# Kernel optimization log

Measured on AMD Instinct MI355X. Metric: run time of the kernel, lower is better.

## Reference

```python
import jax, jax.numpy as jnp
import numpy as np

ALPHA = 0.2  # leakyrelu negative slope

def setup_inputs() -> dict:
    key = jax.random.key(0)
    k1, k2, k3 = jax.random.split(key, 3)
    N, F_in, F_out = 8192, 512, 256
    input_x = jax.random.normal(k1, (N, F_in), dtype=jnp.float32)
    # xavier-ish scaling for params
    W = jax.random.normal(k2, (F_in, F_out), dtype=jnp.float32) * (1.414 * (2.0 / (F_in + F_out)) ** 0.5)
    a = jax.random.normal(k3, (2 * F_out, 1), dtype=jnp.float32) * (1.414 * (2.0 / (2 * F_out + 1)) ** 0.5)
    return {"input_x": input_x, "W": W, "a": a}

def reference(input_x, W, a):
    # h: [N, F_out]
    h = input_x @ W
    F_out = W.shape[1]
    # e_ij = leakyrelu([h_i || h_j] @ a) = leakyrelu(h_i @ a1 + h_j @ a2)
    s1 = h @ a[:F_out, 0]   # [N] contribution of row node i
    s2 = h @ a[F_out:, 0]   # [N] contribution of col node j
    e = jax.nn.leaky_relu(s1[:, None] + s2[None, :], negative_slope=ALPHA)  # [N, N]
    attention = jax.nn.softmax(e, axis=1)
    # dropout p=0.0 (eval) -> identity
    h_prime = attention @ h  # [N, F_out]
    return jax.nn.elu(h_prime)  # concat=True
```

## Files before the change

### kernel.cpp

```cpp
#include <hip/hip_runtime.h>
#include <hip/hip_bf16.h>

#define N_NODES 8192
#define F_IN    512
#define F_OUT   256
#define ALPHA   0.2f
#define CHUNK   32
#define NCHUNK  (N_NODES / CHUNK)
#define SEG     1024

__global__ __launch_bounds__(256) void gemm_h(const float* __restrict__ A,
                                              const float* __restrict__ B,
                                              float* __restrict__ C) {
    __shared__ float As[16][68];
    __shared__ float Bs[16][68];
    const int t  = threadIdx.x;
    const int m0 = blockIdx.y * 64;
    const int n0 = blockIdx.x * 64;

    const int arow = t >> 2;
    const int ac4  = (t & 3) * 4;
    const int brow = t >> 4;
    const int bc4  = (t & 15) * 4;
    const int ty = t >> 4;
    const int tx = t & 15;

    float acc[4][4] = {};

    for (int k0 = 0; k0 < F_IN; k0 += 16) {
        float4 av = *(const float4*)(A + (size_t)(m0 + arow) * F_IN + k0 + ac4);
        float4 bv = *(const float4*)(B + (size_t)(k0 + brow) * F_OUT + n0 + bc4);
        __syncthreads();
        As[ac4 + 0][arow] = av.x;
        As[ac4 + 1][arow] = av.y;
        As[ac4 + 2][arow] = av.z;
        As[ac4 + 3][arow] = av.w;
        *(float4*)(&Bs[brow][bc4]) = bv;
        __syncthreads();
        #pragma unroll
        for (int k = 0; k < 16; ++k) {
            const float4 a4 = *(const float4*)(&As[k][ty * 4]);
            const float4 b4 = *(const float4*)(&Bs[k][tx * 4]);
            acc[0][0] += a4.x * b4.x; acc[0][1] += a4.x * b4.y;
            acc[0][2] += a4.x * b4.z; acc[0][3] += a4.x * b4.w;
            acc[1][0] += a4.y * b4.x; acc[1][1] += a4.y * b4.y;
            acc[1][2] += a4.y * b4.z; acc[1][3] += a4.y * b4.w;
            acc[2][0] += a4.z * b4.x; acc[2][1] += a4.z * b4.y;
            acc[2][2] += a4.z * b4.z; acc[2][3] += a4.z * b4.w;
            acc[3][0] += a4.w * b4.x; acc[3][1] += a4.w * b4.y;
            acc[3][2] += a4.w * b4.z; acc[3][3] += a4.w * b4.w;
        }
    }
    #pragma unroll
    for (int r = 0; r < 4; ++r) {
        float4 o = make_float4(acc[r][0], acc[r][1], acc[r][2], acc[r][3]);
        *(float4*)(C + (size_t)(m0 + ty * 4 + r) * F_OUT + n0 + tx * 4) = o;
    }
}

__global__ __launch_bounds__(256) void s12_kernel(const float* __restrict__ h,
                                                  const float* __restrict__ a,
                                                  float* __restrict__ s1,
                                                  float* __restrict__ s2) {
    const int wave = threadIdx.x >> 6;
    const int lane = threadIdx.x & 63;
    const int row  = blockIdx.x * 4 + wave;

    const float4 hv = *(const float4*)(h + (size_t)row * F_OUT + lane * 4);
    const float4 a1 = *(const float4*)(a + lane * 4);
    const float4 a2 = *(const float4*)(a + F_OUT + lane * 4);

    float p1 = hv.x * a1.x + hv.y * a1.y + hv.z * a1.z + hv.w * a1.w;
    float p2 = hv.x * a2.x + hv.y * a2.y + hv.z * a2.z + hv.w * a2.w;
    #pragma unroll
    for (int off = 32; off; off >>= 1) {
        p1 += __shfl_xor(p1, off);
        p2 += __shfl_xor(p2, off);
    }
    if (lane == 0) { s1[row] = p1; s2[row] = p2; }
}

__global__ __launch_bounds__(1024) void seg_sort(const float* __restrict__ s2,
                                                 float* __restrict__ v,
                                                 int* __restrict__ p) {
    __shared__ float sv[SEG];
    __shared__ int   sp[SEG];
    const int t    = threadIdx.x;
    const int base = blockIdx.x * SEG;
    sv[t] = s2[base + t];
    sp[t] = base + t;
    __syncthreads();
    for (int k = 2; k <= SEG; k <<= 1) {
        for (int j = k >> 1; j > 0; j >>= 1) {
            const int ixj = t ^ j;
            if (ixj > t) {
                const bool up = ((t & k) == 0);
                const float av = sv[t], bv = sv[ixj];
                if (up ? (av > bv) : (av < bv)) {
                    sv[t] = bv; sv[ixj] = av;
                    const int pa = sp[t]; sp[t] = sp[ixj]; sp[ixj] = pa;
                }
            }
            __syncthreads();
        }
    }
    v[base + t] = sv[t];
    p[base + t] = sp[t];
}

__global__ __launch_bounds__(256) void merge_pass(const float* __restrict__ vin,
                                                  const int* __restrict__ pin,
                                                  float* __restrict__ vout,
                                                  int* __restrict__ pout,
                                                  int L) {
    const int gid   = blockIdx.x * 256 + threadIdx.x;
    const int pair  = gid / (2 * L);
    const int local = gid - pair * 2 * L;
    const int beg   = pair * 2 * L;

    if (local < L) {
        const int i     = local;
        const float key = vin[beg + i];
        const int  idx  = pin[beg + i];
        const float* Brun = vin + beg + L;
        int lo = 0, hi = L;
        while (lo < hi) {
            const int mid = (lo + hi) >> 1;
            if (Brun[mid] < key) lo = mid + 1; else hi = mid;
        }
        vout[beg + i + lo] = key;
        pout[beg + i + lo] = idx;
    } else {
        const int i     = local - L;
        const float key = vin[beg + L + i];
        const int  idx  = pin[beg + L + i];
        const float* Arun = vin + beg;
        int lo = 0, hi = L;
        while (lo < hi) {
            const int mid = (lo + hi) >> 1;
            if (Arun[mid] <= key) lo = mid + 1; else hi = mid;
        }
        vout[beg + lo + i] = key;
        pout[beg + lo + i] = idx;
    }
}

__global__ __launch_bounds__(256) void chunk_sums(const float* __restrict__ h,
                                                  const float* __restrict__ v,
                                                  const int* __restrict__ p,
                                                  float* __restrict__ cneg,
                                                  float* __restrict__ cpos,
                                                  float* __restrict__ czn,
                                                  float* __restrict__ czp) {
    const int c = blockIdx.x;
    const int f = threadIdx.x;
    const float M = v[N_NODES - 1];
    float accN = 0.f, accP = 0.f, zn = 0.f, zp = 0.f;
    #pragma unroll 8
    for (int tt = 0; tt < CHUNK; ++tt) {
        const int j = c * CHUNK + tt;
        const float vj = v[j];
        const int pj   = p[j];
        const float wn = __expf(ALPHA * vj);
        const float wp = __expf(vj - M);
        const float hv = h[(size_t)pj * F_OUT + f];
        accN += wn * hv; accP += wp * hv;
        zn += wn; zp += wp;
    }
    cneg[c * F_OUT + f] = accN;
    cpos[c * F_OUT + f] = accP;
    if (f == 0) { czn[c] = zn; czp[c] = zp; }
}

__global__ __launch_bounds__(256) void scan_chunks(float* __restrict__ cneg,
                                                   float* __restrict__ cpos,
                                                   float* __restrict__ czn,
                                                   float* __restrict__ czp) {
    const int f = threadIdx.x;
    float run = 0.f;
    #pragma unroll 4
    for (int c = 0; c < NCHUNK; ++c) {
        const float tv = cneg[c * F_OUT + f];
        cneg[c * F_OUT + f] = run;
        run += tv;
    }
    float runp = 0.f;
    #pragma unroll 4
    for (int c = NCHUNK - 1; c >= 0; --c) {
        const float tv = cpos[c * F_OUT + f];
        cpos[c * F_OUT + f] = runp;
        runp += tv;
    }
    __shared__ float bufn[NCHUNK];
    __shared__ float bufp[NCHUNK];
    const float on = czn[f];
    const float op = czp[f];
    bufn[f] = on;
    bufp[f] = op;
    __syncthreads();
    #pragma unroll
    for (int off = 1; off < NCHUNK; off <<= 1) {
        const float an = (f >= off) ? bufn[f - off] : 0.f;
        const float ap = (f + off < NCHUNK) ? bufp[f + off] : 0.f;
        __syncthreads();
        bufn[f] += an;
        bufp[f] += ap;
        __syncthreads();
    }
    czn[f] = bufn[f] - on;
    czp[f] = bufp[f] - op;
}

__global__ __launch_bounds__(256) void rows2_kernel(const float* __restrict__ s1,
                                                    const float* __restrict__ v,
                                                    const int* __restrict__ p,
                                                    const float* __restrict__ h,
                                                    const float* __restrict__ cnegS,
                                                    const float* __restrict__ cposS,
                                                    const float* __restrict__ cznS,
                                                    const float* __restrict__ czpS,
                                                    float* __restrict__ out) {
    const int wave = threadIdx.x >> 6;
    const int lane = threadIdx.x & 63;
    const int i = blockIdx.x * 4 + wave;

    const float s1v = s1[i];
    const float M   = v[N_NODES - 1];

    const float thr = -s1v;
    int lo = 0, hi = N_NODES;
    while (lo < hi) {
        const int mid = (lo + hi) >> 1;
        if (v[mid] < thr) lo = mid + 1; else hi = mid;
    }
    const int k = lo;
    const int c = min(k >> 5, NCHUNK - 1);
    const int start = c * CHUNK;

    const float4 bN = *(const float4*)(cnegS + (size_t)c * F_OUT + lane * 4);
    const float4 bP = *(const float4*)(cposS + (size_t)c * F_OUT + lane * 4);
    float aN0 = bN.x, aN1 = bN.y, aN2 = bN.z, aN3 = bN.w;
    float aP0 = bP.x, aP1 = bP.y, aP2 = bP.z, aP3 = bP.w;
    float zn = cznS[c];
    float zp = czpS[c];

    #pragma unroll 8
    for (int tt = 0; tt < CHUNK; ++tt) {
        const int j = start + tt;
        const float vj = v[j];
        const int pj   = p[j];
        const float4 hv = *(const float4*)(h + (size_t)pj * F_OUT + lane * 4);
        if (j < k) {
            const float wn = __expf(ALPHA * vj);
            aN0 += wn * hv.x; aN1 += wn * hv.y; aN2 += wn * hv.z; aN3 += wn * hv.w;
            zn += wn;
        } else {
            const float wp = __expf(vj - M);
            aP0 += wp * hv.x; aP1 += wp * hv.y; aP2 += wp * hv.z; aP3 += wp * hv.w;
            zp += wp;
        }
    }

    const float x  = s1v + M;
    const float m  = (x >= 0.f) ? x : ALPHA * x;
    const float cp = __expf(x - m);
    const float cn = __expf(ALPHA * s1v - m);

    const float invZ = 1.0f / (cp * zp + cn * zn);

    float4 o;
    o.x = (cp * aP0 + cn * aN0) * invZ;
    o.y = (cp * aP1 + cn * aN1) * invZ;
    o.z = (cp * aP2 + cn * aN2) * invZ;
    o.w = (cp * aP3 + cn * aN3) * invZ;
    o.x = (o.x > 0.f) ? o.x : expm1f(o.x);
    o.y = (o.y > 0.f) ? o.y : expm1f(o.y);
    o.z = (o.z > 0.f) ? o.z : expm1f(o.z);
    o.w = (o.w > 0.f) ? o.w : expm1f(o.w);
    *(float4*)(out + (size_t)i * F_OUT + lane * 4) = o;
}

__global__ __launch_bounds__(1024) void maxs2_kernel(const float* __restrict__ s2,
                                                     float* __restrict__ M) {
    __shared__ float red[1024];
    float m = -1e30f;
    for (int i = threadIdx.x; i < N_NODES; i += 1024) m = fmaxf(m, s2[i]);
    red[threadIdx.x] = m;
    __syncthreads();
    for (int s = 512; s; s >>= 1) {
        if (threadIdx.x < s) red[threadIdx.x] = fmaxf(red[threadIdx.x], red[threadIdx.x + s]);
        __syncthreads();
    }
    if (threadIdx.x == 0) M[0] = red[0];
}

__global__ __launch_bounds__(256) void aggregate_kernel(const float* __restrict__ h,
                                                        const float* __restrict__ s1,
                                                        const float* __restrict__ s2,
                                                        const float* __restrict__ Mptr,
                                                        float* __restrict__ out) {
    __shared__ float w_lds[32][33];
    __shared__ float s2t[32];
    __shared__ float s1_loc[32];
    __shared__ float m_loc[32];

    const int t  = threadIdx.x;
    const int i0 = blockIdx.x * 32;
    const float Mv = Mptr[0];

    if (t < 32) {
        const float s1v = s1[i0 + t];
        s1_loc[t] = s1v;
        const float x = s1v + Mv;
        m_loc[t] = (x >= 0.f) ? x : ALPHA * x;
    }
    __syncthreads();

    const int g  = t >> 6;
    const int fl = t & 63;
    const int f4 = fl * 4;

    float acc[8][4] = {};
    float zacc[8]   = {};

    for (int j0 = 0; j0 < N_NODES; j0 += 32) {
        __syncthreads();
        if (t < 32) s2t[t] = s2[j0 + t];
        __syncthreads();
        #pragma unroll
        for (int q = 0; q < 4; ++q) {
            const int idx = t + q * 256;
            const int il  = idx >> 5;
            const int jl  = idx & 31;
            float e = s1_loc[il] + s2t[jl];
            e = (e >= 0.f) ? e : ALPHA * e;
            w_lds[il][jl] = __expf(e - m_loc[il]);
        }
        __syncthreads();

        #pragma unroll 4
        for (int jl = 0; jl < 32; ++jl) {
            const float4 hv = *(const float4*)(h + (size_t)(j0 + jl) * F_OUT + f4);
            #pragma unroll
            for (int r = 0; r < 8; ++r) {
                const float w = w_lds[g * 8 + r][jl];
                acc[r][0] += w * hv.x;
                acc[r][1] += w * hv.y;
                acc[r][2] += w * hv.z;
                acc[r][3] += w * hv.w;
                zacc[r]   += w;
            }
        }
    }

    #pragma unroll
    for (int r = 0; r < 8; ++r) {
        const int i = i0 + g * 8 + r;
        const float inv = 1.0f / zacc[r];
        float4 o;
        o.x = acc[r][0] * inv; o.y = acc[r][1] * inv;
        o.z = acc[r][2] * inv; o.w = acc[r][3] * inv;
        o.x = (o.x > 0.f) ? o.x : expm1f(o.x);
        o.y = (o.y > 0.f) ? o.y : expm1f(o.y);
        o.z = (o.z > 0.f) ? o.z : expm1f(o.z);
        o.w = (o.w > 0.f) ? o.w : expm1f(o.w);
        *(float4*)(out + (size_t)i * F_OUT + f4) = o;
    }
}

extern "C" void kernel_launch(void* const* d_in, const int* in_sizes, int n_in,
                              void* d_out, int out_size, void* d_ws, size_t ws_size,
                              hipStream_t stream) {
    const float* x = (const float*)d_in[0];
    const float* W = (const float*)d_in[1];
    const float* a = (const float*)d_in[2];
    float* out = (float*)d_out;

    constexpr size_t SZ_H    = (size_t)N_NODES * F_OUT * 4;
    constexpr size_t SZ_VEC  = (size_t)N_NODES * 4;
    constexpr size_t SZ_CHNK = (size_t)NCHUNK * F_OUT * 4;
    constexpr size_t SZ_CZ   = (size_t)NCHUNK * 4;

    constexpr size_t OFF_H     = 0;
    constexpr size_t OFF_S1    = OFF_H + SZ_H;
    constexpr size_t OFF_S2    = OFF_S1 + SZ_VEC;
    constexpr size_t OFF_V0    = OFF_S2 + SZ_VEC;
    constexpr size_t OFF_P0    = OFF_V0 + SZ_VEC;
    constexpr size_t OFF_V1    = OFF_P0 + SZ_VEC;
    constexpr size_t OFF_P1    = OFF_V1 + SZ_VEC;
    constexpr size_t OFF_CZN   = OFF_P1 + SZ_VEC;
    constexpr size_t OFF_CZP   = OFF_CZN + SZ_CZ;
    constexpr size_t OFF_CNEG  = OFF_CZP + SZ_CZ;
    constexpr size_t OFF_CPOS  = OFF_CNEG + SZ_CHNK;
    constexpr size_t REQUIRED  = OFF_CPOS + SZ_CHNK;

    char* ws = (char*)d_ws;
    float* h  = (float*)(ws + OFF_H);
    float* s1 = (float*)(ws + OFF_S1);
    float* s2 = (float*)(ws + OFF_S2);

    gemm_h<<<dim3(F_OUT / 64, N_NODES / 64), 256, 0, stream>>>(x, W, h);
    s12_kernel<<<N_NODES / 4, 256, 0, stream>>>(h, a, s1, s2);

    if (ws_size >= REQUIRED) {
        float* v0    = (float*)(ws + OFF_V0);
        int*   p0    = (int*)(ws + OFF_P0);
        float* v1    = (float*)(ws + OFF_V1);
        int*   p1    = (int*)(ws + OFF_P1);
        float* czn   = (float*)(ws + OFF_CZN);
        float* czp   = (float*)(ws + OFF_CZP);
        float* cneg  = (float*)(ws + OFF_CNEG);
        float* cpos  = (float*)(ws + OFF_CPOS);

        seg_sort<<<N_NODES / SEG, SEG, 0, stream>>>(s2, v0, p0);
        merge_pass<<<N_NODES / 256, 256, 0, stream>>>(v0, p0, v1, p1, 1024);
        merge_pass<<<N_NODES / 256, 256, 0, stream>>>(v1, p1, v0, p0, 2048);
        merge_pass<<<N_NODES / 256, 256, 0, stream>>>(v0, p0, v1, p1, 4096);

        chunk_sums<<<NCHUNK, 256, 0, stream>>>(h, v1, p1, cneg, cpos, czn, czp);
        scan_chunks<<<1, 256, 0, stream>>>(cneg, cpos, czn, czp);
        rows2_kernel<<<N_NODES / 4, 256, 0, stream>>>(s1, v1, p1, h,
                                                      cneg, cpos, czn, czp, out);
    } else {
        float* M = (float*)(ws + OFF_V0);
        maxs2_kernel<<<1, 1024, 0, stream>>>(s2, M);
        aggregate_kernel<<<N_NODES / 32, 256, 0, stream>>>(h, s1, s2, M, out);
    }
}
```

Before: 198.1 us.

## Parallelize chunk prefix scan across features and prefetch GEMM tiles into registers

The single-block serial scan over 256 chunks per feature becomes a grid of 256 blocks, each doing a shared-memory Hillis-Steele scan over chunks for one feature, with block 0 also scanning the chunk weight totals. This removes a long serial loop of dependent global loads and stores that ran on one workgroup. The GEMM that computes h now uses 128x64 tiles with 512 threads and register prefetch of the next K slice, overlapping global loads with compute. The scan reads and writes are strided by F_OUT, so they are uncoalesced.

```diff
diff --git a/kernel.cpp b/kernel.cpp
--- a/kernel.cpp
+++ b/kernel.cpp
@@ -8,37 +8,47 @@
 #define CHUNK   32
 #define NCHUNK  (N_NODES / CHUNK)
 #define SEG     1024
-
-__global__ __launch_bounds__(256) void gemm_h(const float* __restrict__ A,
+#define BM      128
+#define BN      64
+#define BK      16
+
+__global__ __launch_bounds__(512) void gemm_h(const float* __restrict__ A,
                                               const float* __restrict__ B,
                                               float* __restrict__ C) {
-    __shared__ float As[16][68];
-    __shared__ float Bs[16][68];
+    __shared__ float As[BK][BM + 4];
+    __shared__ float Bs[BK][BN + 4];
     const int t  = threadIdx.x;
-    const int m0 = blockIdx.y * 64;
-    const int n0 = blockIdx.x * 64;
-
-    const int arow = t >> 2;
-    const int ac4  = (t & 3) * 4;
-    const int brow = t >> 4;
-    const int bc4  = (t & 15) * 4;
+    const int m0 = blockIdx.y * BM;
+    const int n0 = blockIdx.x * BN;
+
+    const int ar = t >> 2;
+    const int ak = (t & 3) * 4;
+    const int br = t >> 4;
+    const int bc = (t & 15) * 4;
+
     const int ty = t >> 4;
     const int tx = t & 15;
 
+    float4 aReg = *(const float4*)(A + (size_t)(m0 + ar) * F_IN + ak);
+    float4 bReg = make_float4(0.f, 0.f, 0.f, 0.f);
+    if (t < 256) bReg = *(const float4*)(B + (size_t)br * F_OUT + n0 + bc);
+
     float acc[4][4] = {};
 
-    for (int k0 = 0; k0 < F_IN; k0 += 16) {
-        float4 av = *(const float4*)(A + (size_t)(m0 + arow) * F_IN + k0 + ac4);
-        float4 bv = *(const float4*)(B + (size_t)(k0 + brow) * F_OUT + n0 + bc4);
-        __syncthreads();
-        As[ac4 + 0][arow] = av.x;
-        As[ac4 + 1][arow] = av.y;
-        As[ac4 + 2][arow] = av.z;
-        As[ac4 + 3][arow] = av.w;
-        *(float4*)(&Bs[brow][bc4]) = bv;
-        __syncthreads();
+    for (int k0 = 0; k0 < F_IN; k0 += BK) {
+        __syncthreads();
+        As[ak + 0][ar] = aReg.x;
+        As[ak + 1][ar] = aReg.y;
+        As[ak + 2][ar] = aReg.z;
+        As[ak + 3][ar] = aReg.w;
+        if (t < 256) *(float4*)(&Bs[br][bc]) = bReg;
+        __syncthreads();
+        if (k0 + BK < F_IN) {
+            aReg = *(const float4*)(A + (size_t)(m0 + ar) * F_IN + k0 + BK + ak);
+            if (t < 256) bReg = *(const float4*)(B + (size_t)(k0 + BK + br) * F_OUT + n0 + bc);
+        }
         #pragma unroll
-        for (int k = 0; k < 16; ++k) {
+        for (int k = 0; k < BK; ++k) {
             const float4 a4 = *(const float4*)(&As[k][ty * 4]);
             const float4 b4 = *(const float4*)(&Bs[k][tx * 4]);
             acc[0][0] += a4.x * b4.x; acc[0][1] += a4.x * b4.y;
@@ -172,43 +182,48 @@
     if (f == 0) { czn[c] = zn; czp[c] = zp; }
 }
 
-__global__ __launch_bounds__(256) void scan_chunks(float* __restrict__ cneg,
-                                                   float* __restrict__ cpos,
-                                                   float* __restrict__ czn,
-                                                   float* __restrict__ czp) {
-    const int f = threadIdx.x;
-    float run = 0.f;
-    #pragma unroll 4
-    for (int c = 0; c < NCHUNK; ++c) {
-        const float tv = cneg[c * F_OUT + f];
-        cneg[c * F_OUT + f] = run;
-        run += tv;
-    }
-    float runp = 0.f;
-    #pragma unroll 4
-    for (int c = NCHUNK - 1; c >= 0; --c) {
-        const float tv = cpos[c * F_OUT + f];
-        cpos[c * F_OUT + f] = runp;
-        runp += tv;
-    }
-    __shared__ float bufn[NCHUNK];
-    __shared__ float bufp[NCHUNK];
-    const float on = czn[f];
-    const float op = czp[f];
-    bufn[f] = on;
-    bufp[f] = op;
+__global__ __launch_bounds__(256) void scan_cols(float* __restrict__ cneg,
+                                                 float* __restrict__ cpos,
+                                                 float* __restrict__ czn,
+                                                 float* __restrict__ czp) {
+    const int f = blockIdx.x;
+    const int c = threadIdx.x;
+    __shared__ float bn[NCHUNK];
+    __shared__ float bp[NCHUNK];
+
+    const float xn = cneg[(size_t)c * F_OUT + f];
+    const float xp = cpos[(size_t)c * F_OUT + f];
+    bn[c] = xn; bp[c] = xp;
     __syncthreads();
     #pragma unroll
     for (int off = 1; off < NCHUNK; off <<= 1) {
-        const float an = (f >= off) ? bufn[f - off] : 0.f;
-        const float ap = (f + off < NCHUNK) ? bufp[f + off] : 0.f;
-        __syncthreads();
-        bufn[f] += an;
-        bufp[f] += ap;
-        __syncthreads();
-    }
-    czn[f] = bufn[f] - on;
-    czp[f] = bufp[f] - op;
+        const float an = (c >= off) ? bn[c - off] : 0.f;
+        const float ap = (c + off < NCHUNK) ? bp[c + off] : 0.f;
+        __syncthreads();
+        bn[c] += an; bp[c] += ap;
+        __syncthreads();
+    }
+    cneg[(size_t)c * F_OUT + f] = bn[c] - xn;
+    cpos[(size_t)c * F_OUT + f] = bp[c] - xp;
+
+    if (blockIdx.x == 0) {
+        __shared__ float sn[NCHUNK];
+        __shared__ float sp_[NCHUNK];
+        const float yn = czn[c];
+        const float yp = czp[c];
+        sn[c] = yn; sp_[c] = yp;
+        __syncthreads();
+        #pragma unroll
+        for (int off = 1; off < NCHUNK; off <<= 1) {
+            const float an = (c >= off) ? sn[c - off] : 0.f;
+            const float ap = (c + off < NCHUNK) ? sp_[c + off] : 0.f;
+            __syncthreads();
+            sn[c] += an; sp_[c] += ap;
+            __syncthreads();
+        }
+        czn[c] = sn[c] - yn;
+        czp[c] = sp_[c] - yp;
+    }
 }
 
 __global__ __launch_bounds__(256) void rows2_kernel(const float* __restrict__ s1,
@@ -399,7 +414,7 @@
     float* s1 = (float*)(ws + OFF_S1);
     float* s2 = (float*)(ws + OFF_S2);
 
-    gemm_h<<<dim3(F_OUT / 64, N_NODES / 64), 256, 0, stream>>>(x, W, h);
+    gemm_h<<<dim3(F_OUT / BN, N_NODES / BM), 512, 0, stream>>>(x, W, h);
     s12_kernel<<<N_NODES / 4, 256, 0, stream>>>(h, a, s1, s2);
 
     if (ws_size >= REQUIRED) {
@@ -418,7 +433,7 @@
         merge_pass<<<N_NODES / 256, 256, 0, stream>>>(v0, p0, v1, p1, 4096);
 
         chunk_sums<<<NCHUNK, 256, 0, stream>>>(h, v1, p1, cneg, cpos, czn, czp);
-        scan_chunks<<<1, 256, 0, stream>>>(cneg, cpos, czn, czp);
+        scan_cols<<<F_OUT, NCHUNK, 0, stream>>>(cneg, cpos, czn, czp);
         rows2_kernel<<<N_NODES / 4, 256, 0, stream>>>(s1, v1, p1, h,
                                                       cneg, cpos, czn, czp, out);
     } else {
```

New measurement: 164.0 us. 17.2% less time.
